# Kernel tuning notes

Hardware: AMD Instinct MI355X
Metric: run time of the kernel (lower is better)

Reference implementation:

```python
import jax, jax.numpy as jnp
import numpy as np

B, S, H, NH = 2, 2048, 4096, 32
HD = H // NH  # head_dim = 128
ROPE_BASE = 10000.0


def setup_inputs() -> dict:
    key = jax.random.key(0)
    k1, k2, k3 = jax.random.split(key, 3)
    hidden_states = jax.random.normal(k1, (B, S, H), dtype=jnp.float32)
    w_qkv = jax.random.normal(k2, (H, 3 * H), dtype=jnp.float32) * 0.02
    w_o = jax.random.normal(k3, (H, H), dtype=jnp.float32) * 0.02
    position_ids = jnp.broadcast_to(jnp.arange(S, dtype=jnp.int32), (B, S))
    return {"hidden_states": hidden_states, "w_qkv": w_qkv, "w_o": w_o,
            "position_ids": position_ids}


def _rope_neox(x, cos, sin):
    # x: [B,S,NH,HD]; cos/sin: [B,S,1,HD//2]. NeoX rotate-halves.
    half = HD // 2
    x1, x2 = x[..., :half], x[..., half:]
    return jnp.concatenate([x1 * cos - x2 * sin, x2 * cos + x1 * sin], axis=-1)


def reference(hidden_states, w_qkv, w_o, position_ids):
    # fused QKV projection (stands in for quantized WQLinear)
    qkv = hidden_states @ w_qkv                        # [B,S,3H]
    q, k, v = jnp.split(qkv, 3, axis=-1)
    q = q.reshape(B, S, NH, HD)
    k = k.reshape(B, S, NH, HD)
    v = v.reshape(B, S, NH, HD)

    # NeoX rotary embedding indexed by position_ids
    inv_freq = 1.0 / (ROPE_BASE ** (jnp.arange(0, HD, 2, dtype=jnp.float32) / HD))
    freqs = position_ids.astype(jnp.float32)[..., None] * inv_freq  # [B,S,HD/2]
    cos = jnp.cos(freqs)[:, :, None, :]
    sin = jnp.sin(freqs)[:, :, None, :]
    q = _rope_neox(q, cos, sin)
    k = _rope_neox(k, cos, sin)

    # causal SDPA (prefill path: past_key_value is None -> is_causal=True)
    scale = 1.0 / jnp.sqrt(jnp.asarray(HD, dtype=q.dtype))
    scores = jnp.einsum('bqhd,bkhd->bhqk', q, k) * scale  # [B,NH,S,S]
    causal = jnp.tril(jnp.ones((S, S), dtype=bool))
    scores = jnp.where(causal, scores, jnp.finfo(scores.dtype).min)
    probs = jax.nn.softmax(scores, axis=-1)
    attn = jnp.einsum('bhqk,bkhd->bqhd', probs, v).reshape(B, S, H)

    return attn @ w_o  # [B,S,H]
```

## Files before the change

### kernel.cpp

```cpp
#include <hip/hip_runtime.h>
#include <stdint.h>
#include <math.h>

#define B_ 2
#define S_ 2048
#define H_ 4096
#define NH_ 32
#define HD_ 128

using s16x8 = __attribute__((ext_vector_type(8))) short;
using f32x4 = __attribute__((ext_vector_type(4))) float;

__device__ __forceinline__ unsigned short f2b(float f) {
  union { float f; unsigned u; } v; v.f = f;
  unsigned r = v.u + 0x7FFFu + ((v.u >> 16) & 1u);
  return (unsigned short)(r >> 16);
}
__device__ __forceinline__ unsigned short f2b_trunc(float f) {
  union { float f; unsigned u; } v; v.f = f;
  return (unsigned short)(v.u >> 16);
}
__device__ __forceinline__ float b2f(unsigned short h) {
  union { unsigned u; float f; } v; v.u = ((unsigned)h) << 16;
  return v.f;
}

__device__ __forceinline__ void async_cp16(const void* g, void* l) {
  __builtin_amdgcn_global_load_lds(
      (__attribute__((address_space(1))) void*)(void*)g,
      (__attribute__((address_space(3))) void*)l, 16, 0, 0);
}

#define MFMA16(a, b, c) __builtin_amdgcn_mfma_f32_16x16x32_bf16((a), (b), (c), 0, 0, 0)
#define BARRIER() asm volatile("s_barrier" ::: "memory")

__global__ void cast_f32_bf16(const float* __restrict__ in,
                              unsigned short* __restrict__ out, long n) {
  long i = ((long)blockIdx.x * 256 + threadIdx.x) * 4;
  if (i >= n) return;
  const float4 v = *(const float4*)(in + i);
  ushort4 o;
  o.x = f2b(v.x); o.y = f2b(v.y); o.z = f2b(v.z); o.w = f2b(v.w);
  *(ushort4*)(out + i) = o;
}

__global__ void transpose_cast_4096(const float* __restrict__ in,
                                    unsigned short* __restrict__ out, int in_stride) {
  __shared__ float tile[64][65];
  const int c0 = blockIdx.x * 64;
  const int r0 = blockIdx.y * 64;
  const int tx = threadIdx.x & 63, ty = threadIdx.x >> 6;
#pragma unroll
  for (int i = 0; i < 64; i += 4)
    tile[ty + i][tx] = in[(long)(r0 + ty + i) * in_stride + c0 + tx];
  __syncthreads();
#pragma unroll
  for (int i = 0; i < 64; i += 4)
    out[(long)(c0 + ty + i) * 4096 + r0 + tx] = f2b(tile[tx][ty + i]);
}

template <int MODE>
__global__ __launch_bounds__(512, 2) void gemm_bt(
    const unsigned short* __restrict__ A,
    const unsigned short* __restrict__ Bt,
    float* __restrict__ Cf,
    unsigned short* __restrict__ Dst,
    int M, int N, int K) {
  __shared__ __align__(16) unsigned short lds[65536];
  const int tid = threadIdx.x;
  const int lane = tid & 63;
  const int w = tid >> 6;
  const int quad = lane >> 4, l16 = lane & 15;
  const int wm = w >> 2, wn = w & 3;

  const int id = blockIdx.x;
  const int swz = (id & 7) * 32 + (id >> 3);
  const int m0 = (swz >> 4) * 256;
  const int n0 = (swz & 15) * 256;

  const int lr = tid >> 3;
  const int c8 = (tid & 7) * 8;
  const int csw = c8 ^ (((lr >> 1) & 7) << 3);
  const unsigned short* gA = A + (long)(m0 + lr) * K + csw;
  const unsigned short* gB = Bt + (long)(n0 + lr) * K + csw;
  const long K64 = (long)K * 64;
  const int ldsS = lr * 64 + c8;

  const int fsw = ((l16 >> 1) & 7) << 3;
  const int colk0 = (quad * 8) ^ fsw;
  const int colk1 = colk0 ^ 32;
  const int aoff0 = (wm * 128 + l16) * 64 + colk0;
  const int aoff1 = (wm * 128 + l16) * 64 + colk1;
  const int boff0 = 32768 + (wn * 64 + l16) * 64 + colk0;
  const int boff1 = 32768 + (wn * 64 + l16) * 64 + colk1;

  const f32x4 z4 = {0.f, 0.f, 0.f, 0.f};
  f32x4 acc[8][4];
#pragma unroll
  for (int mi = 0; mi < 8; mi++)
#pragma unroll
    for (int ni = 0; ni < 4; ni++) acc[mi][ni] = z4;

  async_cp16(gB, &lds[32768 + ldsS]);
  async_cp16(gB + K64, &lds[32768 + ldsS + 4096]);
  async_cp16(gB + 2 * K64, &lds[32768 + 8192 + ldsS]);
  async_cp16(gB + 3 * K64, &lds[32768 + 8192 + ldsS + 4096]);
  async_cp16(gA, &lds[ldsS]);
  async_cp16(gA + K64, &lds[ldsS + 4096]);
  async_cp16(gA + 2 * K64, &lds[8192 + ldsS]);
  async_cp16(gA + 3 * K64, &lds[8192 + ldsS + 4096]);
  async_cp16(gB + 64, &lds[32768 + 16384 + ldsS]);
  async_cp16(gB + 64 + K64, &lds[32768 + 16384 + ldsS + 4096]);
  async_cp16(gB + 64 + 2 * K64, &lds[32768 + 16384 + 8192 + ldsS]);
  async_cp16(gB + 64 + 3 * K64, &lds[32768 + 16384 + 8192 + ldsS + 4096]);
  asm volatile("s_waitcnt vmcnt(4)\n\ts_barrier" ::: "memory");

  const int NT = 64;
  for (int t = 0; t < NT; ++t) {
    const int buf = (t & 1) * 16384;
    const int nbuf = 16384 - buf;
    const long kA = (long)(t + 1) * 64;
    const long kB = (long)(t + 2) * 64;
    s16x8 a1[4][2], a2[4][2], b0[2][2], b1[2][2];

#pragma unroll
    for (int mi = 0; mi < 4; ++mi) {
      a1[mi][0] = *(const s16x8*)&lds[buf + aoff0 + mi * 1024];
      a1[mi][1] = *(const s16x8*)&lds[buf + aoff1 + mi * 1024];
    }
#pragma unroll
    for (int ni = 0; ni < 2; ++ni) {
      b0[ni][0] = *(const s16x8*)&lds[buf + boff0 + ni * 1024];
      b0[ni][1] = *(const s16x8*)&lds[buf + boff1 + ni * 1024];
    }
#pragma unroll
    for (int ni = 0; ni < 2; ++ni) {
      b1[ni][0] = *(const s16x8*)&lds[buf + boff0 + (ni + 2) * 1024];
      b1[ni][1] = *(const s16x8*)&lds[buf + boff1 + (ni + 2) * 1024];
    }
#pragma unroll
    for (int mi = 0; mi < 4; ++mi) {
      a2[mi][0] = *(const s16x8*)&lds[buf + aoff0 + (mi + 4) * 1024];
      a2[mi][1] = *(const s16x8*)&lds[buf + aoff1 + (mi + 4) * 1024];
    }
    if (t < NT - 1) {
      async_cp16(gA + kA, &lds[nbuf + ldsS]);
      async_cp16(gA + kA + K64, &lds[nbuf + ldsS + 4096]);
    }
    BARRIER();
    __builtin_amdgcn_s_setprio(1);
#pragma unroll
    for (int mi = 0; mi < 4; ++mi)
#pragma unroll
      for (int ni = 0; ni < 2; ++ni) {
        acc[mi][ni] = MFMA16(a1[mi][0], b0[ni][0], acc[mi][ni]);
        acc[mi][ni] = MFMA16(a1[mi][1], b0[ni][1], acc[mi][ni]);
      }
    __builtin_amdgcn_s_setprio(0);
    BARRIER();

    if (t < NT - 1) {
      async_cp16(gA + kA + 2 * K64, &lds[nbuf + 8192 + ldsS]);
      async_cp16(gA + kA + 3 * K64, &lds[nbuf + 8192 + ldsS + 4096]);
    }
    BARRIER();
    __builtin_amdgcn_s_setprio(1);
#pragma unroll
    for (int mi = 0; mi < 4; ++mi)
#pragma unroll
      for (int ni = 0; ni < 2; ++ni) {
        acc[mi][ni + 2] = MFMA16(a1[mi][0], b1[ni][0], acc[mi][ni + 2]);
        acc[mi][ni + 2] = MFMA16(a1[mi][1], b1[ni][1], acc[mi][ni + 2]);
      }
    __builtin_amdgcn_s_setprio(0);
    BARRIER();

    if (t < NT - 2) {
      async_cp16(gB + kB, &lds[32768 + buf + ldsS]);
      async_cp16(gB + kB + K64, &lds[32768 + buf + ldsS + 4096]);
    }
    BARRIER();
    __builtin_amdgcn_s_setprio(1);
#pragma unroll
    for (int mi = 0; mi < 4; ++mi)
#pragma unroll
      for (int ni = 0; ni < 2; ++ni) {
        acc[mi + 4][ni + 2] = MFMA16(a2[mi][0], b1[ni][0], acc[mi + 4][ni + 2]);
        acc[mi + 4][ni + 2] = MFMA16(a2[mi][1], b1[ni][1], acc[mi + 4][ni + 2]);
      }
    __builtin_amdgcn_s_setprio(0);
    BARRIER();

    if (t < NT - 2) {
      async_cp16(gB + kB + 2 * K64, &lds[32768 + buf + 8192 + ldsS]);
      async_cp16(gB + kB + 3 * K64, &lds[32768 + buf + 8192 + ldsS + 4096]);
    }
    BARRIER();
    __builtin_amdgcn_s_setprio(1);
#pragma unroll
    for (int mi = 0; mi < 4; ++mi)
#pragma unroll
      for (int ni = 0; ni < 2; ++ni) {
        acc[mi + 4][ni] = MFMA16(a2[mi][0], b0[ni][0], acc[mi + 4][ni]);
        acc[mi + 4][ni] = MFMA16(a2[mi][1], b0[ni][1], acc[mi + 4][ni]);
      }
    __builtin_amdgcn_s_setprio(0);
    if (t < NT - 2) {
      asm volatile("s_waitcnt vmcnt(4)\n\ts_barrier" ::: "memory");
    } else if (t == NT - 2) {
      asm volatile("s_waitcnt vmcnt(0)\n\ts_barrier" ::: "memory");
    } else {
      BARRIER();
    }
  }

#pragma unroll
  for (int mi = 0; mi < 8; ++mi)
#pragma unroll
    for (int ni = 0; ni < 4; ++ni) {
      const int row = m0 + wm * 128 + mi * 16 + quad * 4;
      const int col = n0 + wn * 64 + ni * 16 + l16;
      if (MODE == 0) {
#pragma unroll
        for (int r = 0; r < 4; ++r)
          Cf[(long)(row + r) * N + col] = acc[mi][ni][r];
      } else {
        const int h = col >> 7, d = col & 127;
#pragma unroll
        for (int r = 0; r < 4; ++r) {
          const int m = row + r;
          const int b = m >> 11, s = m & 2047;
          Dst[((long)((b * NH_ + h) * S_) + s) * HD_ + d] = f2b(acc[mi][ni][r]);
        }
      }
    }
}

__global__ void rope_kernel(unsigned short* __restrict__ Qb,
                            unsigned short* __restrict__ Kb,
                            const int* __restrict__ pos_ids) {
  const float QSCALE = 1.4426950408889634f * 0.08838834764831845f;
  const long idx = (long)blockIdx.x * 256 + threadIdx.x;
  const int i = (int)(idx & 63);
  const long row = idx >> 6;
  const int s = (int)(row & (S_ - 1));
  const long bh = row >> 11;
  const int b = (int)(bh >> 5);
  const float pos = (float)pos_ids[b * S_ + s];
  const float inv = exp2f(-(float)i * 0.20762050593046f);
  const float ang = pos * inv;
  const float sn = sinf(ang), cs = cosf(ang);
  const long base = row * HD_;
  const float q1 = b2f(Qb[base + i]), q2 = b2f(Qb[base + 64 + i]);
  Qb[base + i] = f2b((q1 * cs - q2 * sn) * QSCALE);
  Qb[base + 64 + i] = f2b((q2 * cs + q1 * sn) * QSCALE);
  const float k1 = b2f(Kb[base + i]), k2 = b2f(Kb[base + 64 + i]);
  Kb[base + i] = f2b(k1 * cs - k2 * sn);
  Kb[base + 64 + i] = f2b(k2 * cs + k1 * sn);
}

__global__ void transpose_v(const unsigned short* __restrict__ V,
                            unsigned short* __restrict__ Vt) {
  __shared__ unsigned short tile[64][66];
  const int bh = blockIdx.z;
  const int s0 = blockIdx.x * 64;
  const int d0 = blockIdx.y * 64;
  const unsigned short* src = V + (long)bh * S_ * HD_;
  unsigned short* dst = Vt + (long)bh * S_ * HD_;
  const int tx = threadIdx.x & 63, ty = threadIdx.x >> 6;
#pragma unroll
  for (int i = 0; i < 64; i += 4)
    tile[ty + i][tx] = src[(long)(s0 + ty + i) * HD_ + d0 + tx];
  __syncthreads();
#pragma unroll
  for (int i = 0; i < 64; i += 4)
    dst[(long)(d0 + ty + i) * S_ + s0 + tx] = tile[tx][ty + i];
}

__global__ __launch_bounds__(256, 2) void flash_attn(
    const unsigned short* __restrict__ Qb,
    const unsigned short* __restrict__ Kb,
    const unsigned short* __restrict__ Vt,
    unsigned short* __restrict__ Ab) {
  __shared__ __align__(16) unsigned short Ks[16 * 64 * 8];
  __shared__ __align__(16) unsigned short Vs[8 * 128 * 8];
  __shared__ __align__(16) unsigned short plds[128 * 72];
  const int tid = threadIdx.x;
  const int w = tid >> 6, lane = tid & 63;
  const int quad = lane >> 4, l16 = lane & 15;
  const int qx = blockIdx.y;
  const int bh = blockIdx.x;
  const int b = bh >> 5, h = bh & 31;

  const unsigned short* Qh = Qb + (long)bh * S_ * HD_;
  const unsigned short* Kh = Kb + (long)bh * S_ * HD_;
  const unsigned short* Vh = Vt + (long)bh * S_ * HD_;

  const unsigned short* kstage = Kh + (long)(tid & 63) * HD_ + (tid >> 6) * 8;
  const unsigned short* vstage = Vh + (long)(tid & 127) * S_ + (tid >> 7) * 8;

  const f32x4 z4 = {0.f, 0.f, 0.f, 0.f};
  s16x8 onesv;
#pragma unroll
  for (int j = 0; j < 8; j++) onesv[j] = (short)0x3F80;

  for (int half = 0; half < 2; half++) {
    const int qt = half ? qx : 15 - qx;
    const int q0 = qt * 128;
    const int wq = q0 + w * 32;

    s16x8 qf[2][4];
#pragma unroll
    for (int rb = 0; rb < 2; rb++)
#pragma unroll
      for (int ks = 0; ks < 4; ks++)
        qf[rb][ks] = *(const s16x8*)(Qh + (long)(wq + rb * 16 + l16) * HD_ + ks * 32 + quad * 8);

    f32x4 oacc[2][8];
    f32x4 lacc[2];
#pragma unroll
    for (int rb = 0; rb < 2; rb++) {
#pragma unroll
      for (int oc = 0; oc < 8; oc++) oacc[rb][oc] = z4;
      lacc[rb] = z4;
    }
    float mrow[2][4];
#pragma unroll
    for (int rb = 0; rb < 2; rb++)
#pragma unroll
      for (int r = 0; r < 4; r++) mrow[rb][r] = -3.0e38f;

    const int nkt = 2 * qt + 2;

    for (int kt = 0; kt < nkt; kt++) {
      const int kbase = kt * 64;
      __syncthreads();
#pragma unroll
      for (int j = 0; j < 4; j++)
        async_cp16(kstage + (long)kbase * HD_ + j * 32, &Ks[(j * 256 + tid) * 8]);
#pragma unroll
      for (int j = 0; j < 4; j++)
        async_cp16(vstage + kbase + j * 16, &Vs[(j * 256 + tid) * 8]);
      __syncthreads();

      const bool active = (kbase < wq + 32);
      if (active) {
        f32x4 sacc[2][4];
#pragma unroll
        for (int rb = 0; rb < 2; rb++)
#pragma unroll
          for (int ni = 0; ni < 4; ni++) sacc[rb][ni] = z4;
        __builtin_amdgcn_s_setprio(1);
#pragma unroll
        for (int ni = 0; ni < 4; ni++) {
#pragma unroll
          for (int ks = 0; ks < 4; ks++) {
            const s16x8 kf = *(const s16x8*)&Ks[((ks * 4 + quad) * 64 + ni * 16 + l16) * 8];
            sacc[0][ni] = MFMA16(qf[0][ks], kf, sacc[0][ni]);
            sacc[1][ni] = MFMA16(qf[1][ks], kf, sacc[1][ni]);
          }
        }
        __builtin_amdgcn_s_setprio(0);

        const bool band = (kbase + 64 > wq);
        float pm[2][4];
        bool small_ = true;
#pragma unroll
        for (int rb = 0; rb < 2; rb++) {
          const int rloc = w * 32 + rb * 16 + quad * 4;
          if (band) {
#pragma unroll
            for (int ni = 0; ni < 4; ni++)
#pragma unroll
              for (int r = 0; r < 4; r++)
                if (kbase + ni * 16 + l16 > q0 + rloc + r) sacc[rb][ni][r] = -3.0e38f;
          }
#pragma unroll
          for (int r = 0; r < 4; r++) {
            pm[rb][r] = fmaxf(fmaxf(sacc[rb][0][r], sacc[rb][1][r]),
                              fmaxf(sacc[rb][2][r], sacc[rb][3][r]));
            small_ = small_ && (pm[rb][r] <= mrow[rb][r] + 8.0f);
          }
        }
        const bool nores = __all(small_);

        if (!nores) {
#pragma unroll
          for (int rb = 0; rb < 2; rb++) {
            float alpha[4];
#pragma unroll
            for (int r = 0; r < 4; r++) {
              float m = pm[rb][r];
#pragma unroll
              for (int off = 1; off < 16; off <<= 1) m = fmaxf(m, __shfl_xor(m, off));
              const float mn = fmaxf(mrow[rb][r], m);
              alpha[r] = __builtin_amdgcn_exp2f(mrow[rb][r] - mn);
              mrow[rb][r] = mn;
            }
#pragma unroll
            for (int oc = 0; oc < 8; oc++)
#pragma unroll
              for (int r = 0; r < 4; r++) oacc[rb][oc][r] *= alpha[r];
#pragma unroll
            for (int r = 0; r < 4; r++) lacc[rb][r] *= alpha[r];
          }
        }

#pragma unroll
        for (int rb = 0; rb < 2; rb++) {
          const int rloc = w * 32 + rb * 16 + quad * 4;
#pragma unroll
          for (int ni = 0; ni < 4; ni++)
#pragma unroll
            for (int r = 0; r < 4; r++) {
              const float p = __builtin_amdgcn_exp2f(sacc[rb][ni][r] - mrow[rb][r]);
              plds[(rloc + r) * 72 + ni * 16 + l16] = f2b_trunc(p);
            }
        }

        s16x8 af[2][2];
#pragma unroll
        for (int rb = 0; rb < 2; rb++)
#pragma unroll
          for (int ks = 0; ks < 2; ks++)
            af[rb][ks] = *(const s16x8*)&plds[(w * 32 + rb * 16 + l16) * 72 + ks * 32 + quad * 8];
        __builtin_amdgcn_s_setprio(1);
#pragma unroll
        for (int rb = 0; rb < 2; rb++) {
          lacc[rb] = MFMA16(af[rb][0], onesv, lacc[rb]);
          lacc[rb] = MFMA16(af[rb][1], onesv, lacc[rb]);
        }
#pragma unroll
        for (int oc = 0; oc < 8; oc++) {
#pragma unroll
          for (int ks = 0; ks < 2; ks++) {
            const s16x8 vf = *(const s16x8*)&Vs[((ks * 4 + quad) * 128 + oc * 16 + l16) * 8];
            oacc[0][oc] = MFMA16(af[0][ks], vf, oacc[0][oc]);
            oacc[1][oc] = MFMA16(af[1][ks], vf, oacc[1][oc]);
          }
        }
        __builtin_amdgcn_s_setprio(0);
      }
    }

#pragma unroll
    for (int rb = 0; rb < 2; rb++) {
      float inv_l[4];
#pragma unroll
      for (int r = 0; r < 4; r++) inv_l[r] = 1.f / lacc[rb][r];
#pragma unroll
      for (int oc = 0; oc < 8; oc++)
#pragma unroll
        for (int r = 0; r < 4; r++) {
          const int s = q0 + w * 32 + rb * 16 + quad * 4 + r;
          const int d = oc * 16 + l16;
          Ab[((long)(b * S_ + s)) * H_ + h * HD_ + d] = f2b(oacc[rb][oc][r] * inv_l[r]);
        }
    }
  }
}

extern "C" void kernel_launch(void* const* d_in, const int* in_sizes, int n_in,
                              void* d_out, int out_size, void* d_ws, size_t ws_size,
                              hipStream_t stream) {
  const float* hs = (const float*)d_in[0];
  const float* w_qkv = (const float*)d_in[1];
  const float* w_o = (const float*)d_in[2];
  const int* pos = (const int*)d_in[3];
  float* out = (float*)d_out;

  const long EL = (long)4096 * 4096;
  unsigned short* Xb = (unsigned short*)d_ws;
  unsigned short* Wt = Xb + EL;
  unsigned short* Qb = Wt + EL;
  unsigned short* Kb = Qb + EL;
  unsigned short* Vb = Kb + EL;
  unsigned short* Vt = Vb + EL;
  unsigned short* Ab = Xb;

  cast_f32_bf16<<<(EL / 4 + 255) / 256, 256, 0, stream>>>(hs, Xb, EL);

  unsigned short* qkv_dst[3] = {Qb, Kb, Vb};
  for (int p = 0; p < 3; p++) {
    transpose_cast_4096<<<dim3(64, 64), 256, 0, stream>>>(w_qkv + p * 4096, Wt, 12288);
    gemm_bt<1><<<dim3(256), dim3(512), 0, stream>>>(Xb, Wt, nullptr, qkv_dst[p], 4096, 4096, 4096);
  }

  rope_kernel<<<(B_ * NH_ * S_ * 64) / 256, 256, 0, stream>>>(Qb, Kb, pos);
  transpose_v<<<dim3(32, 2, 64), 256, 0, stream>>>(Vb, Vt);
  flash_attn<<<dim3(64, 8), 256, 0, stream>>>(Qb, Kb, Vt, Ab);

  transpose_cast_4096<<<dim3(64, 64), 256, 0, stream>>>(w_o, Wt, 4096);
  gemm_bt<0><<<dim3(256), dim3(512), 0, stream>>>(Ab, Wt, out, nullptr, 4096, 4096, 4096);
}
```

Baseline: 968.0 us.

## Vectorize weight transpose-cast, merge GEMM phases, prefetch K/V in flash attention

The weight transpose-cast now packs two bf16 values per 32-bit LDS word and uses float4 loads and 16-byte stores, replacing scalar accesses. The GEMM main loop merges its four barrier-separated MFMA phases into two, issuing all A and B async copies together to cut the number of barriers per K step. Flash attention double-buffers V in LDS and issues the next tile's K/V async copies right after the QK^T MFMAs, so the loads overlap the softmax and PV work. The price is more LDS, a wider live register set in the GEMM, and new ordering hazards around the reused K buffer.

```diff
diff --git a/kernel.cpp b/kernel.cpp
--- a/kernel.cpp
+++ b/kernel.cpp
@@ -46,17 +46,32 @@
 
 __global__ void transpose_cast_4096(const float* __restrict__ in,
                                     unsigned short* __restrict__ out, int in_stride) {
-  __shared__ float tile[64][65];
+  __shared__ unsigned tile[64][33];
+  const int t = threadIdx.x;
   const int c0 = blockIdx.x * 64;
   const int r0 = blockIdx.y * 64;
-  const int tx = threadIdx.x & 63, ty = threadIdx.x >> 6;
-#pragma unroll
-  for (int i = 0; i < 64; i += 4)
-    tile[ty + i][tx] = in[(long)(r0 + ty + i) * in_stride + c0 + tx];
+  const int l16 = t & 15, q = t >> 4;
+  const int c4 = l16 * 4;
+#pragma unroll
+  for (int ii = 0; ii < 2; ii++) {
+    const int p = q + ii * 16;
+    const float4 ra = *(const float4*)&in[(long)(r0 + 2 * p) * in_stride + c0 + c4];
+    const float4 rb = *(const float4*)&in[(long)(r0 + 2 * p + 1) * in_stride + c0 + c4];
+    tile[c4 + 0][p] = (unsigned)f2b(ra.x) | ((unsigned)f2b(rb.x) << 16);
+    tile[c4 + 1][p] = (unsigned)f2b(ra.y) | ((unsigned)f2b(rb.y) << 16);
+    tile[c4 + 2][p] = (unsigned)f2b(ra.z) | ((unsigned)f2b(rb.z) << 16);
+    tile[c4 + 3][p] = (unsigned)f2b(ra.w) | ((unsigned)f2b(rb.w) << 16);
+  }
   __syncthreads();
-#pragma unroll
-  for (int i = 0; i < 64; i += 4)
-    out[(long)(c0 + ty + i) * 4096 + r0 + tx] = f2b(tile[tx][ty + i]);
+  const int c = t >> 2, r8 = (t & 3) * 8;
+  unsigned v[8];
+#pragma unroll
+  for (int k = 0; k < 8; k++) v[k] = tile[c][r8 + k];
+  uint4 o0 = {v[0], v[1], v[2], v[3]};
+  uint4 o1 = {v[4], v[5], v[6], v[7]};
+  unsigned short* dst = &out[(long)(c0 + c) * 4096 + r0 + 2 * r8];
+  *(uint4*)dst = o0;
+  *(uint4*)(dst + 8) = o1;
 }
 
 template <int MODE>
@@ -132,22 +147,15 @@
     for (int ni = 0; ni < 2; ++ni) {
       b0[ni][0] = *(const s16x8*)&lds[buf + boff0 + ni * 1024];
       b0[ni][1] = *(const s16x8*)&lds[buf + boff1 + ni * 1024];
-    }
-#pragma unroll
-    for (int ni = 0; ni < 2; ++ni) {
       b1[ni][0] = *(const s16x8*)&lds[buf + boff0 + (ni + 2) * 1024];
       b1[ni][1] = *(const s16x8*)&lds[buf + boff1 + (ni + 2) * 1024];
-    }
-#pragma unroll
-    for (int mi = 0; mi < 4; ++mi) {
-      a2[mi][0] = *(const s16x8*)&lds[buf + aoff0 + (mi + 4) * 1024];
-      a2[mi][1] = *(const s16x8*)&lds[buf + aoff1 + (mi + 4) * 1024];
     }
     if (t < NT - 1) {
       async_cp16(gA + kA, &lds[nbuf + ldsS]);
       async_cp16(gA + kA + K64, &lds[nbuf + ldsS + 4096]);
-    }
-    BARRIER();
+      async_cp16(gA + kA + 2 * K64, &lds[nbuf + 8192 + ldsS]);
+      async_cp16(gA + kA + 3 * K64, &lds[nbuf + 8192 + ldsS + 4096]);
+    }
     __builtin_amdgcn_s_setprio(1);
 #pragma unroll
     for (int mi = 0; mi < 4; ++mi)
@@ -155,47 +163,23 @@
       for (int ni = 0; ni < 2; ++ni) {
         acc[mi][ni] = MFMA16(a1[mi][0], b0[ni][0], acc[mi][ni]);
         acc[mi][ni] = MFMA16(a1[mi][1], b0[ni][1], acc[mi][ni]);
-      }
-    __builtin_amdgcn_s_setprio(0);
-    BARRIER();
-
-    if (t < NT - 1) {
-      async_cp16(gA + kA + 2 * K64, &lds[nbuf + 8192 + ldsS]);
-      async_cp16(gA + kA + 3 * K64, &lds[nbuf + 8192 + ldsS + 4096]);
-    }
-    BARRIER();
-    __builtin_amdgcn_s_setprio(1);
-#pragma unroll
-    for (int mi = 0; mi < 4; ++mi)
-#pragma unroll
-      for (int ni = 0; ni < 2; ++ni) {
         acc[mi][ni + 2] = MFMA16(a1[mi][0], b1[ni][0], acc[mi][ni + 2]);
         acc[mi][ni + 2] = MFMA16(a1[mi][1], b1[ni][1], acc[mi][ni + 2]);
       }
     __builtin_amdgcn_s_setprio(0);
-    BARRIER();
-
+    asm volatile("s_waitcnt lgkmcnt(0)\n\ts_barrier" ::: "memory");
+
+#pragma unroll
+    for (int mi = 0; mi < 4; ++mi) {
+      a2[mi][0] = *(const s16x8*)&lds[buf + aoff0 + (mi + 4) * 1024];
+      a2[mi][1] = *(const s16x8*)&lds[buf + aoff1 + (mi + 4) * 1024];
+    }
     if (t < NT - 2) {
       async_cp16(gB + kB, &lds[32768 + buf + ldsS]);
       async_cp16(gB + kB + K64, &lds[32768 + buf + ldsS + 4096]);
-    }
-    BARRIER();
-    __builtin_amdgcn_s_setprio(1);
-#pragma unroll
-    for (int mi = 0; mi < 4; ++mi)
-#pragma unroll
-      for (int ni = 0; ni < 2; ++ni) {
-        acc[mi + 4][ni + 2] = MFMA16(a2[mi][0], b1[ni][0], acc[mi + 4][ni + 2]);
-        acc[mi + 4][ni + 2] = MFMA16(a2[mi][1], b1[ni][1], acc[mi + 4][ni + 2]);
-      }
-    __builtin_amdgcn_s_setprio(0);
-    BARRIER();
-
-    if (t < NT - 2) {
       async_cp16(gB + kB + 2 * K64, &lds[32768 + buf + 8192 + ldsS]);
       async_cp16(gB + kB + 3 * K64, &lds[32768 + buf + 8192 + ldsS + 4096]);
     }
-    BARRIER();
     __builtin_amdgcn_s_setprio(1);
 #pragma unroll
     for (int mi = 0; mi < 4; ++mi)
@@ -203,6 +187,8 @@
       for (int ni = 0; ni < 2; ++ni) {
         acc[mi + 4][ni] = MFMA16(a2[mi][0], b0[ni][0], acc[mi + 4][ni]);
         acc[mi + 4][ni] = MFMA16(a2[mi][1], b0[ni][1], acc[mi + 4][ni]);
+        acc[mi + 4][ni + 2] = MFMA16(a2[mi][0], b1[ni][0], acc[mi + 4][ni + 2]);
+        acc[mi + 4][ni + 2] = MFMA16(a2[mi][1], b1[ni][1], acc[mi + 4][ni + 2]);
       }
     __builtin_amdgcn_s_setprio(0);
     if (t < NT - 2) {
@@ -283,7 +269,7 @@
     const unsigned short* __restrict__ Vt,
     unsigned short* __restrict__ Ab) {
   __shared__ __align__(16) unsigned short Ks[16 * 64 * 8];
-  __shared__ __align__(16) unsigned short Vs[8 * 128 * 8];
+  __shared__ __align__(16) unsigned short Vs[2][8 * 128 * 8];
   __shared__ __align__(16) unsigned short plds[128 * 72];
   const int tid = threadIdx.x;
   const int w = tid >> 6, lane = tid & 63;
@@ -304,6 +290,15 @@
 #pragma unroll
   for (int j = 0; j < 8; j++) onesv[j] = (short)0x3F80;
 
+#pragma unroll
+  for (int j = 0; j < 4; j++)
+    async_cp16(kstage + j * 32, &Ks[(j * 256 + tid) * 8]);
+#pragma unroll
+  for (int j = 0; j < 4; j++)
+    async_cp16(vstage + j * 16, &Vs[0][(j * 256 + tid) * 8]);
+  asm volatile("s_waitcnt vmcnt(0)" ::: "memory");
+  __syncthreads();
+
   for (int half = 0; half < 2; half++) {
     const int qt = half ? qx : 15 - qx;
     const int q0 = qt * 128;
@@ -334,18 +329,11 @@
 
     for (int kt = 0; kt < nkt; kt++) {
       const int kbase = kt * 64;
-      __syncthreads();
-#pragma unroll
-      for (int j = 0; j < 4; j++)
-        async_cp16(kstage + (long)kbase * HD_ + j * 32, &Ks[(j * 256 + tid) * 8]);
-#pragma unroll
-      for (int j = 0; j < 4; j++)
-        async_cp16(vstage + kbase + j * 16, &Vs[(j * 256 + tid) * 8]);
-      __syncthreads();
-
+      const int cur = kt & 1;
       const bool active = (kbase < wq + 32);
+
+      f32x4 sacc[2][4];
       if (active) {
-        f32x4 sacc[2][4];
 #pragma unroll
         for (int rb = 0; rb < 2; rb++)
 #pragma unroll
@@ -361,7 +349,21 @@
           }
         }
         __builtin_amdgcn_s_setprio(0);
-
+      }
+      __syncthreads();
+
+      const bool more = (kt + 1 < nkt);
+      if (more || half == 0) {
+        const long nkb = more ? (long)(kbase + 64) : 0;
+#pragma unroll
+        for (int j = 0; j < 4; j++)
+          async_cp16(kstage + nkb * HD_ + j * 32, &Ks[(j * 256 + tid) * 8]);
+#pragma unroll
+        for (int j = 0; j < 4; j++)
+          async_cp16(vstage + nkb + j * 16, &Vs[1 - cur][(j * 256 + tid) * 8]);
+      }
+
+      if (active) {
         const bool band = (kbase + 64 > wq);
         float pm[2][4];
         bool small_ = true;
@@ -434,13 +436,16 @@
         for (int oc = 0; oc < 8; oc++) {
 #pragma unroll
           for (int ks = 0; ks < 2; ks++) {
-            const s16x8 vf = *(const s16x8*)&Vs[((ks * 4 + quad) * 128 + oc * 16 + l16) * 8];
+            const s16x8 vf = *(const s16x8*)&Vs[cur][((ks * 4 + quad) * 128 + oc * 16 + l16) * 8];
             oacc[0][oc] = MFMA16(af[0][ks], vf, oacc[0][oc]);
             oacc[1][oc] = MFMA16(af[1][ks], vf, oacc[1][oc]);
           }
         }
         __builtin_amdgcn_s_setprio(0);
       }
+
+      asm volatile("s_waitcnt vmcnt(0)" ::: "memory");
+      __syncthreads();
     }
 
 #pragma unroll
```

Result: no change. 950.9 us (-1.8%).
